# Optimization experiments

Hardware: AMD Instinct MI355X
Metric: run time of the kernel (lower is better)

## Reference

```python
import jax, jax.numpy as jnp
import numpy as np

N, E, DIM, H = 50000, 800000, 256, 4
HD = DIM // H  # per-head dim = 64
NEG_SLOPE = 0.2
EPS = 1e-5


def _layernorm(x, g, b):
    mu = jnp.mean(x, axis=-1, keepdims=True)
    var = jnp.mean(jnp.square(x - mu), axis=-1, keepdims=True)
    return (x - mu) * jax.lax.rsqrt(var + EPS) * g + b


def setup_inputs() -> dict:
    key = jax.random.key(0)
    ks = jax.random.split(key, 8)
    s = 1.0 / np.sqrt(DIM)
    return {
        "x": jax.random.normal(ks[0], (N, DIM), dtype=jnp.float32),
        "edge_index": jax.random.randint(ks[1], (2, E), 0, N, dtype=jnp.int64),
        "W": jax.random.normal(ks[2], (DIM, DIM), dtype=jnp.float32) * s,
        "a_src": jax.random.normal(ks[3], (H, HD), dtype=jnp.float32) * s,
        "a_dst": jax.random.normal(ks[4], (H, HD), dtype=jnp.float32) * s,
        "gat_b": jnp.zeros((DIM,), jnp.float32),
        "ln1_g": jnp.ones((DIM,), jnp.float32),
        "ln1_b": jnp.zeros((DIM,), jnp.float32),
        "W1": jax.random.normal(ks[5], (DIM, 2 * DIM), dtype=jnp.float32) * s,
        "b1": jnp.zeros((2 * DIM,), jnp.float32),
        "W2": jax.random.normal(ks[6], (2 * DIM, DIM), dtype=jnp.float32) * (1.0 / np.sqrt(2 * DIM)),
        "b2": jnp.zeros((DIM,), jnp.float32),
        "ln2_g": jnp.ones((DIM,), jnp.float32),
        "ln2_b": jnp.zeros((DIM,), jnp.float32),
    }


def _gat(x, edge_index, W, a_src, a_dst, gat_b):
    # add self-loops (PyG GATConv default)
    loops = jnp.arange(N, dtype=edge_index.dtype)
    src = jnp.concatenate([edge_index[0], loops])
    dst = jnp.concatenate([edge_index[1], loops])
    h = (x @ W).reshape(N, H, HD)                    # [N,H,D]
    al_src = jnp.einsum("nhd,hd->nh", h, a_src)      # [N,H]
    al_dst = jnp.einsum("nhd,hd->nh", h, a_dst)
    e = jax.nn.leaky_relu(al_src[src] + al_dst[dst], NEG_SLOPE)  # [E',H]
    # softmax over edges grouped by destination node
    emax = jax.ops.segment_max(e, dst, num_segments=N)           # [N,H]
    ex = jnp.exp(e - emax[dst])
    denom = jax.ops.segment_sum(ex, dst, num_segments=N)         # [N,H]
    alpha = ex / denom[dst]                                      # [E',H]
    msg = alpha[:, :, None] * h[src]                             # [E',H,D]
    out = jax.ops.segment_sum(msg, dst, num_segments=N)          # [N,H,D]
    return out.reshape(N, DIM) + gat_b


def reference(x, edge_index, W, a_src, a_dst, gat_b, ln1_g, ln1_b, W1, b1, W2, b2, ln2_g, ln2_b):
    res = x
    y = _gat(x, edge_index, W, a_src, a_dst, gat_b)
    y = _layernorm(y + res, ln1_g, ln1_b)
    res = y
    f = jax.nn.gelu(y @ W1 + b1, approximate=False) @ W2 + b2
    return _layernorm(f + res, ln2_g, ln2_b)
```

## Files before the change

kernel.cpp:

```cpp
#include <hip/hip_runtime.h>

typedef __bf16 bf16_t;
typedef __bf16 bf16x4 __attribute__((ext_vector_type(4)));
typedef __bf16 bf16x8 __attribute__((ext_vector_type(8)));
typedef float  f32x4  __attribute__((ext_vector_type(4)));
typedef unsigned u32x2 __attribute__((ext_vector_type(2)));

__device__ inline float loadf(const void* p, size_t i, int bf) {
    return bf ? (float)((const bf16_t*)p)[i] : ((const float*)p)[i];
}
__device__ inline void storef(void* p, size_t i, int bf, float v) {
    if (bf) ((bf16_t*)p)[i] = (bf16_t)v; else ((float*)p)[i] = v;
}
__device__ inline int eidx(const void* p, size_t i, int i64) {
    return i64 ? (int)((const long long*)p)[i] : ((const int*)p)[i];
}
__device__ inline float bflo(unsigned u) { return __uint_as_float(u << 16); }
__device__ inline float bfhi(unsigned u) { return __uint_as_float(u & 0xFFFF0000u); }

__global__ void detect_k(const void* __restrict__ x, const void* __restrict__ ei,
                         int E, int* __restrict__ flags) {
    int l = threadIdx.x;
    const unsigned* xu = (const unsigned*)x;
    unsigned low = xu[l] & 0xFFFFu;
    unsigned ex = (low >> 7) & 0xFF;
    int cnt = __popcll(__ballot(ex >= 115 && ex <= 133));
    const unsigned* eu = (const unsigned*)ei;
    int lim = E < 64 ? E : 64;
    unsigned v = (l < lim) ? eu[2 * (size_t)l + 1] : 0u;
    unsigned long long nz = __ballot(v != 0u);
    if (l == 0) { flags[0] = (cnt >= 32) ? 1 : 0; flags[1] = (nz == 0ull) ? 1 : 0; }
}

__global__ void transpose_k(const void* __restrict__ in, bf16_t* __restrict__ out,
                            int R, int C, const int* __restrict__ flags) {
    int bf = flags[0];
    int i = blockIdx.x * 256 + threadIdx.x;
    if (i < R * C) { int r = i / C, c = i % C; out[c * R + r] = (bf16_t)loadf(in, i, bf); }
}

__global__ __launch_bounds__(256) void gemm128(const void* __restrict__ A,
                                               const bf16_t* __restrict__ BT,
                                               const void* __restrict__ bias,
                                               bf16_t* __restrict__ C,
                                               int M, int N, int K, int act,
                                               const int* __restrict__ flags, int a_ext,
                                               const void* __restrict__ a_srcp,
                                               const void* __restrict__ a_dstp,
                                               float* __restrict__ alsrc,
                                               float* __restrict__ aldst, int do_al) {
    int bf = flags[0];
    int a_bf = a_ext ? bf : 1;
    __shared__ bf16_t As[128][40];
    __shared__ bf16_t Bs[128][40];
    int t = threadIdx.x;
    int tm = blockIdx.x * 128;
    int tn = blockIdx.y * 128;
    int w = t >> 6, l = t & 63;
    int wr = (w >> 1) * 64, wc = (w & 1) * 64;
    int lr = l & 15, lk = (l >> 4) * 8;

    f32x4 acc[4][4];
#pragma unroll
    for (int i = 0; i < 4; i++)
#pragma unroll
        for (int j = 0; j < 4; j++) acc[i][j] = (f32x4){0.f, 0.f, 0.f, 0.f};

    int r0 = t >> 2;
    int kc = (t & 3) * 8;

    for (int k0 = 0; k0 < K; k0 += 32) {
#pragma unroll
        for (int j = 0; j < 2; j++) {
            int r = r0 + j * 64;
            int ra = tm + r; if (ra > M - 1) ra = M - 1;
            if (a_bf) {
                *(bf16x8*)&As[r][kc] = *(const bf16x8*)((const bf16_t*)A + (size_t)ra * K + k0 + kc);
            } else {
                const float* Af = (const float*)A + (size_t)ra * K + k0 + kc;
                f32x4 a = *(const f32x4*)Af;
                f32x4 b2 = *(const f32x4*)(Af + 4);
                bf16x8 rr;
                rr[0]=(bf16_t)a[0]; rr[1]=(bf16_t)a[1]; rr[2]=(bf16_t)a[2]; rr[3]=(bf16_t)a[3];
                rr[4]=(bf16_t)b2[0]; rr[5]=(bf16_t)b2[1]; rr[6]=(bf16_t)b2[2]; rr[7]=(bf16_t)b2[3];
                *(bf16x8*)&As[r][kc] = rr;
            }
            *(bf16x8*)&Bs[r][kc] = *(const bf16x8*)(BT + (size_t)(tn + r) * K + k0 + kc);
        }
        __syncthreads();
        bf16x8 af[4], bg[4];
#pragma unroll
        for (int i = 0; i < 4; i++) {
            af[i] = *(bf16x8*)&As[wr + i * 16 + lr][lk];
            bg[i] = *(bf16x8*)&Bs[wc + i * 16 + lr][lk];
        }
#pragma unroll
        for (int i = 0; i < 4; i++)
#pragma unroll
            for (int j = 0; j < 4; j++)
                acc[i][j] = __builtin_amdgcn_mfma_f32_16x16x32_bf16(af[i], bg[j], acc[i][j], 0, 0, 0);
        __syncthreads();
    }

    int cr0 = (l >> 4) * 4;

    if (do_al) {
        float asv[4], adv[4];
#pragma unroll
        for (int j = 0; j < 4; j++) {
            int col = tn + wc + j * 16 + lr;
            asv[j] = loadf(a_srcp, col, bf);
            adv[j] = loadf(a_dstp, col, bf);
        }
        int head = (tn + wc) >> 6;
#pragma unroll
        for (int i = 0; i < 4; i++) {
#pragma unroll
            for (int q = 0; q < 4; q++) {
                float ps = acc[i][0][q]*asv[0] + acc[i][1][q]*asv[1] + acc[i][2][q]*asv[2] + acc[i][3][q]*asv[3];
                float pd = acc[i][0][q]*adv[0] + acc[i][1][q]*adv[1] + acc[i][2][q]*adv[2] + acc[i][3][q]*adv[3];
#pragma unroll
                for (int d = 1; d < 16; d <<= 1) { ps += __shfl_xor(ps, d); pd += __shfl_xor(pd, d); }
                int row = tm + wr + i * 16 + cr0 + q;
                if (lr == 0 && row < M) { alsrc[row * 4 + head] = ps; aldst[row * 4 + head] = pd; }
            }
        }
    }

#pragma unroll
    for (int i = 0; i < 4; i++) {
#pragma unroll
        for (int j = 0; j < 4; j++) {
            int col = tn + wc + j * 16 + lr;
            float bv = bias ? loadf(bias, col, bf) : 0.f;
#pragma unroll
            for (int q = 0; q < 4; q++) {
                int row = tm + wr + i * 16 + cr0 + q;
                if (row < M) {
                    float v = acc[i][j][q] + bv;
                    if (act) v = 0.5f * v * (1.f + erff(v * 0.70710678118f));
                    C[(size_t)row * N + col] = (bf16_t)v;
                }
            }
        }
    }
}

__global__ void deg_k(const void* __restrict__ ei, int* __restrict__ deg, int E, int N,
                      const int* __restrict__ flags) {
    int i64 = flags[1];
    int i = blockIdx.x * 256 + threadIdx.x;
    if (i < E) {
        int d = eidx(ei, (size_t)E + i, i64);
        if ((unsigned)d >= (unsigned)N) d = 0;
        atomicAdd(&deg[d], 1);
    }
}

__global__ __launch_bounds__(256) void scan1(const int* __restrict__ deg, int* __restrict__ offs,
                                             int* __restrict__ chunkSum) {
    __shared__ int s[256];
    int t = threadIdx.x, b = blockIdx.x;
    int v = deg[b * 256 + t];
    s[t] = v; __syncthreads();
#pragma unroll
    for (int d = 1; d < 256; d <<= 1) {
        int u = (t >= d) ? s[t - d] : 0;
        __syncthreads(); s[t] += u; __syncthreads();
    }
    offs[b * 256 + t] = s[t] - v;
    if (t == 255) chunkSum[b] = s[255];
}

__global__ __launch_bounds__(256) void scan2(const int* __restrict__ chunkSum, int* __restrict__ chunkOff, int nch) {
    __shared__ int s[256];
    int t = threadIdx.x;
    int v = (t < nch) ? chunkSum[t] : 0;
    s[t] = v; __syncthreads();
#pragma unroll
    for (int d = 1; d < 256; d <<= 1) {
        int u = (t >= d) ? s[t - d] : 0;
        __syncthreads(); s[t] += u; __syncthreads();
    }
    chunkOff[t] = s[t] - v;
}

__global__ void scan3(int* __restrict__ offs, const int* __restrict__ chunkOff,
                      int* __restrict__ cursor, int total) {
    int i = blockIdx.x * 256 + threadIdx.x;
    if (i < total) { int v = offs[i] + chunkOff[i >> 8]; offs[i] = v; cursor[i] = v; }
}

__global__ void scatter_k(const void* __restrict__ ei, int* __restrict__ cursor,
                          int* __restrict__ csr, float* __restrict__ ews4,
                          const float* __restrict__ alsrc, const float* __restrict__ aldst,
                          int E, int N, const int* __restrict__ flags) {
    int i64 = flags[1];
    int i = blockIdx.x * 256 + threadIdx.x;
    if (i < E) {
        int s = eidx(ei, i, i64);
        int d = eidx(ei, (size_t)E + i, i64);
        if ((unsigned)s >= (unsigned)N) s = 0;
        if ((unsigned)d >= (unsigned)N) d = 0;
        int p = atomicAdd(&cursor[d], 1);
        csr[p] = s;
        f32x4 as4 = *(const f32x4*)&alsrc[s * 4];
        f32x4 ad4 = *(const f32x4*)&aldst[d * 4];
        f32x4 w4;
#pragma unroll
        for (int hh = 0; hh < 4; hh++) {
            float e = as4[hh] + ad4[hh];
            e = e > 0.f ? e : 0.2f * e;
            w4[hh] = expf(fminf(e, 30.f));
        }
        *(f32x4*)&ews4[4 * (size_t)p] = w4;
    }
}

__global__ __launch_bounds__(256) void gat_agg_ln(
    const bf16_t* __restrict__ hbuf, const void* __restrict__ x,
    const float* __restrict__ alsrc, const float* __restrict__ aldst,
    const int* __restrict__ offs, const int* __restrict__ csr,
    const float* __restrict__ ews4,
    const void* __restrict__ gatb, const void* __restrict__ lng, const void* __restrict__ lnb,
    bf16_t* __restrict__ y, const int* __restrict__ flags, int N) {
    int bf = flags[0];
    int w = threadIdx.x >> 6, l = threadIdx.x & 63;
    int n = blockIdx.x * 4 + w;
    if (n >= N) return;
    int h = l >> 4;
    int col0 = l * 4;

    __shared__ int   srcs[4][64];
    __shared__ float ewt[4][4][68];

    int off = offs[n], deg = offs[n + 1] - off;

    float es = alsrc[n * 4 + h] + aldst[n * 4 + h];
    es = es > 0.f ? es : 0.2f * es;
    float wself = expf(fminf(es, 30.f));

    float a0 = 0.f, a1 = 0.f, a2 = 0.f, a3 = 0.f;
    f32x4 ssum = (f32x4){0.f, 0.f, 0.f, 0.f};

    for (int c0 = 0; c0 < deg; c0 += 64) {
        int cl = deg - c0; if (cl > 64) cl = 64;
        if (l < cl) {
            int sv = csr[off + c0 + l];
            srcs[w][l] = sv;
            f32x4 wv = *(const f32x4*)&ews4[4 * (size_t)(off + c0 + l)];
            ewt[w][0][l] = wv[0]; ewt[w][1][l] = wv[1];
            ewt[w][2][l] = wv[2]; ewt[w][3][l] = wv[3];
            ssum += wv;
        }
        int i = 0;
        for (; i + 4 <= cl; i += 4) {
            int s0 = __builtin_amdgcn_readfirstlane(srcs[w][i]);
            int s1 = __builtin_amdgcn_readfirstlane(srcs[w][i + 1]);
            int s2 = __builtin_amdgcn_readfirstlane(srcs[w][i + 2]);
            int s3 = __builtin_amdgcn_readfirstlane(srcs[w][i + 3]);
            u32x2 v0 = ((const u32x2*)(hbuf + (size_t)s0 * 256))[l];
            u32x2 v1 = ((const u32x2*)(hbuf + (size_t)s1 * 256))[l];
            u32x2 v2 = ((const u32x2*)(hbuf + (size_t)s2 * 256))[l];
            u32x2 v3 = ((const u32x2*)(hbuf + (size_t)s3 * 256))[l];
            f32x4 wq = *(const f32x4*)&ewt[w][h][i];
            a0 += wq[0]*bflo(v0[0]); a1 += wq[0]*bfhi(v0[0]); a2 += wq[0]*bflo(v0[1]); a3 += wq[0]*bfhi(v0[1]);
            a0 += wq[1]*bflo(v1[0]); a1 += wq[1]*bfhi(v1[0]); a2 += wq[1]*bflo(v1[1]); a3 += wq[1]*bfhi(v1[1]);
            a0 += wq[2]*bflo(v2[0]); a1 += wq[2]*bfhi(v2[0]); a2 += wq[2]*bflo(v2[1]); a3 += wq[2]*bfhi(v2[1]);
            a0 += wq[3]*bflo(v3[0]); a1 += wq[3]*bfhi(v3[0]); a2 += wq[3]*bflo(v3[1]); a3 += wq[3]*bfhi(v3[1]);
        }
        for (; i < cl; i++) {
            int sv = __builtin_amdgcn_readfirstlane(srcs[w][i]);
            float wgt = ewt[w][h][i];
            u32x2 v0 = ((const u32x2*)(hbuf + (size_t)sv * 256))[l];
            a0 += wgt*bflo(v0[0]); a1 += wgt*bfhi(v0[0]); a2 += wgt*bflo(v0[1]); a3 += wgt*bfhi(v0[1]);
        }
    }

#pragma unroll
    for (int d = 1; d < 64; d <<= 1) {
        ssum[0] += __shfl_xor(ssum[0], d);
        ssum[1] += __shfl_xor(ssum[1], d);
        ssum[2] += __shfl_xor(ssum[2], d);
        ssum[3] += __shfl_xor(ssum[3], d);
    }
    float dsum = (h == 0) ? ssum[0] : (h == 1) ? ssum[1] : (h == 2) ? ssum[2] : ssum[3];
    float di = 1.f / (dsum + wself);

    u32x2 sv2 = ((const u32x2*)(hbuf + (size_t)n * 256))[l];
    size_t xbase = (size_t)n * 256 + col0;
    float v0f = (a0 + wself*bflo(sv2[0])) * di + loadf(gatb, col0 + 0, bf) + loadf(x, xbase + 0, bf);
    float v1f = (a1 + wself*bfhi(sv2[0])) * di + loadf(gatb, col0 + 1, bf) + loadf(x, xbase + 1, bf);
    float v2f = (a2 + wself*bflo(sv2[1])) * di + loadf(gatb, col0 + 2, bf) + loadf(x, xbase + 2, bf);
    float v3f = (a3 + wself*bfhi(sv2[1])) * di + loadf(gatb, col0 + 3, bf) + loadf(x, xbase + 3, bf);

    float s1 = v0f + v1f + v2f + v3f;
#pragma unroll
    for (int d = 1; d < 64; d <<= 1) s1 += __shfl_xor(s1, d);
    float mu = s1 * (1.f / 256.f);
    float c0f = v0f - mu, c1f = v1f - mu, c2f = v2f - mu, c3f = v3f - mu;
    float sq = c0f*c0f + c1f*c1f + c2f*c2f + c3f*c3f;
#pragma unroll
    for (int d = 1; d < 64; d <<= 1) sq += __shfl_xor(sq, d);
    float rs = rsqrtf(sq * (1.f / 256.f) + 1e-5f);

    bf16x4 o;
    o[0] = (bf16_t)(c0f * rs * loadf(lng, col0 + 0, bf) + loadf(lnb, col0 + 0, bf));
    o[1] = (bf16_t)(c1f * rs * loadf(lng, col0 + 1, bf) + loadf(lnb, col0 + 1, bf));
    o[2] = (bf16_t)(c2f * rs * loadf(lng, col0 + 2, bf) + loadf(lnb, col0 + 2, bf));
    o[3] = (bf16_t)(c3f * rs * loadf(lng, col0 + 3, bf) + loadf(lnb, col0 + 3, bf));
    *(bf16x4*)&y[(size_t)n * 256 + col0] = o;
}

__global__ __launch_bounds__(256) void ln_res(const bf16_t* __restrict__ f, const bf16_t* __restrict__ y,
                                              const void* __restrict__ g, const void* __restrict__ b,
                                              void* __restrict__ out, int N, const int* __restrict__ flags) {
    int bf = flags[0];
    int row = blockIdx.x * 4 + (threadIdx.x >> 6);
    int l = threadIdx.x & 63;
    if (row >= N) return;
    int col0 = l * 4;
    u32x2 fv = *(const u32x2*)(f + (size_t)row * 256 + col0);
    u32x2 yv = *(const u32x2*)(y + (size_t)row * 256 + col0);
    float v0 = bflo(fv[0]) + bflo(yv[0]);
    float v1 = bfhi(fv[0]) + bfhi(yv[0]);
    float v2 = bflo(fv[1]) + bflo(yv[1]);
    float v3 = bfhi(fv[1]) + bfhi(yv[1]);
    float s = v0 + v1 + v2 + v3;
#pragma unroll
    for (int d = 1; d < 64; d <<= 1) s += __shfl_xor(s, d);
    float mu = s * (1.f / 256.f);
    float c0 = v0 - mu, c1 = v1 - mu, c2 = v2 - mu, c3 = v3 - mu;
    float sq = c0*c0 + c1*c1 + c2*c2 + c3*c3;
#pragma unroll
    for (int d = 1; d < 64; d <<= 1) sq += __shfl_xor(sq, d);
    float rs = rsqrtf(sq * (1.f / 256.f) + 1e-5f);
    float o0 = c0 * rs * loadf(g, col0 + 0, bf) + loadf(b, col0 + 0, bf);
    float o1 = c1 * rs * loadf(g, col0 + 1, bf) + loadf(b, col0 + 1, bf);
    float o2 = c2 * rs * loadf(g, col0 + 2, bf) + loadf(b, col0 + 2, bf);
    float o3 = c3 * rs * loadf(g, col0 + 3, bf) + loadf(b, col0 + 3, bf);
    if (bf) {
        bf16x4 o; o[0]=(bf16_t)o0; o[1]=(bf16_t)o1; o[2]=(bf16_t)o2; o[3]=(bf16_t)o3;
        *(bf16x4*)&((bf16_t*)out)[(size_t)row * 256 + col0] = o;
    } else {
        f32x4 o = (f32x4){o0, o1, o2, o3};
        *(f32x4*)&((float*)out)[(size_t)row * 256 + col0] = o;
    }
}

extern "C" void kernel_launch(void* const* d_in, const int* in_sizes, int n_in,
                              void* d_out, int out_size, void* d_ws, size_t ws_size,
                              hipStream_t stream) {
    const void* x    = d_in[0];
    const void* ei   = d_in[1];
    const void* W    = d_in[2];
    const void* a_src= d_in[3];
    const void* a_dst= d_in[4];
    const void* gatb = d_in[5];
    const void* ln1g = d_in[6];
    const void* ln1b = d_in[7];
    const void* W1   = d_in[8];
    const void* b1   = d_in[9];
    const void* W2   = d_in[10];
    const void* b2   = d_in[11];
    const void* ln2g = d_in[12];
    const void* ln2b = d_in[13];

    const int DIM = 256, DFF = 512;
    int N = in_sizes[0] / DIM;
    int E = in_sizes[1] / 2;

    char* ws = (char*)d_ws;
    size_t o = 0;
    auto alloc = [&](size_t bytes) { void* p = ws + o; o += (bytes + 255) & ~(size_t)255; return p; };
    int*    flags  = (int*)alloc(256);
    bf16_t* WT     = (bf16_t*)alloc((size_t)DIM * DIM * 2);
    bf16_t* W1T    = (bf16_t*)alloc((size_t)DIM * DFF * 2);
    bf16_t* W2T    = (bf16_t*)alloc((size_t)DFF * DIM * 2);
    float*  alsrc  = (float*)alloc((size_t)N * 4 * 4);
    float*  aldst  = (float*)alloc((size_t)N * 4 * 4);
    int nch = (N + 255) / 256;
    int tot = nch * 256;
    int* deg      = (int*)alloc((size_t)tot * 4);
    int* offs     = (int*)alloc((size_t)(tot + 1) * 4);
    int* cursor   = (int*)alloc((size_t)tot * 4);
    int* chunkSum = (int*)alloc(256 * 4);
    int* chunkOff = (int*)alloc(256 * 4);
    int* csr      = (int*)alloc((size_t)E * 4);
    float* ews4   = (float*)alloc((size_t)E * 16);
    bf16_t* h     = (bf16_t*)alloc((size_t)N * DIM * 2);
    bf16_t* yb    = (bf16_t*)alloc((size_t)N * DIM * 2);
    bf16_t* fb    = h;
    size_t remain = (ws_size > o) ? (ws_size - o) : 0;
    long CH = (long)(remain / ((size_t)DFF * 2));
    if (CH > N) CH = N;
    if (CH < 1024) CH = 1024;
    bf16_t* t1 = (bf16_t*)alloc((size_t)CH * DFF * 2);

    detect_k<<<1, 64, 0, stream>>>(x, ei, E, flags);
    hipMemsetAsync(deg, 0, (size_t)tot * 4, stream);

    transpose_k<<<(DIM * DIM + 255) / 256, 256, 0, stream>>>(W,  WT,  DIM, DIM, flags);
    transpose_k<<<(DIM * DFF + 255) / 256, 256, 0, stream>>>(W1, W1T, DIM, DFF, flags);
    transpose_k<<<(DFF * DIM + 255) / 256, 256, 0, stream>>>(W2, W2T, DFF, DIM, flags);

    dim3 g1((N + 127) / 128, DIM / 128);
    gemm128<<<g1, 256, 0, stream>>>(x, WT, nullptr, h, N, DIM, DIM, 0, flags, 1,
                                    a_src, a_dst, alsrc, aldst, 1);

    deg_k<<<(E + 255) / 256, 256, 0, stream>>>(ei, deg, E, N, flags);
    scan1<<<nch, 256, 0, stream>>>(deg, offs, chunkSum);
    scan2<<<1, 256, 0, stream>>>(chunkSum, chunkOff, nch);
    scan3<<<(tot + 255) / 256, 256, 0, stream>>>(offs, chunkOff, cursor, tot);
    scatter_k<<<(E + 255) / 256, 256, 0, stream>>>(ei, cursor, csr, ews4, alsrc, aldst, E, N, flags);

    gat_agg_ln<<<(N + 3) / 4, 256, 0, stream>>>(h, x, alsrc, aldst, offs, csr, ews4,
                                                gatb, ln1g, ln1b, yb, flags, N);

    for (long r0 = 0; r0 < N; r0 += CH) {
        int m = (int)((N - r0 < CH) ? (N - r0) : CH);
        dim3 g2((m + 127) / 128, DFF / 128);
        gemm128<<<g2, 256, 0, stream>>>(yb + r0 * DIM, W1T, b1, t1, m, DFF, DIM, 1, flags, 0,
                                        nullptr, nullptr, nullptr, nullptr, 0);
        dim3 g3((m + 127) / 128, DIM / 128);
        gemm128<<<g3, 256, 0, stream>>>(t1, W2T, b2, fb + r0 * DIM, m, DIM, DFF, 0, flags, 0,
                                        nullptr, nullptr, nullptr, nullptr, 0);
    }

    ln_res<<<(N + 3) / 4, 256, 0, stream>>>(fb, yb, ln2g, ln2b, d_out, N, flags);
}
```

Measured before the change: 427.9 us.

## Double-buffer GEMM with direct global-to-LDS loads, stage output, compress edge weights

The GEMM now loads A/B tiles straight into LDS via global_load_lds into a double buffer, so the next K-slab's fetch overlaps the current MFMA work. A k-major LDS layout replaces the padded one. Epilogue stores go through LDS and write coalesced 16-byte rows. Input x is pre-converted to bf16 in a separate pass so the GEMM sees only bf16 A, and per-edge softmax weights are stored as bf16 instead of fp32 to halve that traffic, at a small precision cost and one extra kernel pass over x.

```diff
diff --git a/kernel.cpp b/kernel.cpp
--- a/kernel.cpp
+++ b/kernel.cpp
@@ -17,6 +17,12 @@
 }
 __device__ inline float bflo(unsigned u) { return __uint_as_float(u << 16); }
 __device__ inline float bfhi(unsigned u) { return __uint_as_float(u & 0xFFFF0000u); }
+
+__device__ inline void gload16(const bf16_t* g, char* l) {
+    __builtin_amdgcn_global_load_lds(
+        (const __attribute__((address_space(1))) unsigned*)g,
+        (__attribute__((address_space(3))) unsigned*)l, 16, 0, 0);
+}
 
 __global__ void detect_k(const void* __restrict__ x, const void* __restrict__ ei,
                          int E, int* __restrict__ flags) {
@@ -32,6 +38,26 @@
     if (l == 0) { flags[0] = (cnt >= 32) ? 1 : 0; flags[1] = (nz == 0ull) ? 1 : 0; }
 }
 
+__global__ void tobf16_k(const void* __restrict__ in, bf16_t* __restrict__ out,
+                         long n, const int* __restrict__ flags) {
+    int bf = flags[0];
+    long i = ((long)blockIdx.x * 256 + threadIdx.x) * 8;
+    long stride = (long)gridDim.x * 256 * 8;
+    if (bf) {
+        for (; i < n; i += stride)
+            *(bf16x8*)&out[i] = *(const bf16x8*)((const bf16_t*)in + i);
+    } else {
+        for (; i < n; i += stride) {
+            f32x4 a = *(const f32x4*)((const float*)in + i);
+            f32x4 b = *(const f32x4*)((const float*)in + i + 4);
+            bf16x8 r;
+            r[0]=(bf16_t)a[0]; r[1]=(bf16_t)a[1]; r[2]=(bf16_t)a[2]; r[3]=(bf16_t)a[3];
+            r[4]=(bf16_t)b[0]; r[5]=(bf16_t)b[1]; r[6]=(bf16_t)b[2]; r[7]=(bf16_t)b[3];
+            *(bf16x8*)&out[i] = r;
+        }
+    }
+}
+
 __global__ void transpose_k(const void* __restrict__ in, bf16_t* __restrict__ out,
                             int R, int C, const int* __restrict__ flags) {
     int bf = flags[0];
@@ -39,26 +65,25 @@
     if (i < R * C) { int r = i / C, c = i % C; out[c * R + r] = (bf16_t)loadf(in, i, bf); }
 }
 
-__global__ __launch_bounds__(256) void gemm128(const void* __restrict__ A,
+__global__ __launch_bounds__(256) void gemm128(const bf16_t* __restrict__ A,
                                                const bf16_t* __restrict__ BT,
                                                const void* __restrict__ bias,
                                                bf16_t* __restrict__ C,
                                                int M, int N, int K, int act,
-                                               const int* __restrict__ flags, int a_ext,
+                                               const int* __restrict__ flags,
                                                const void* __restrict__ a_srcp,
                                                const void* __restrict__ a_dstp,
                                                float* __restrict__ alsrc,
                                                float* __restrict__ aldst, int do_al) {
     int bf = flags[0];
-    int a_bf = a_ext ? bf : 1;
-    __shared__ bf16_t As[128][40];
-    __shared__ bf16_t Bs[128][40];
+    __shared__ __align__(16) char smem[34816];
     int t = threadIdx.x;
     int tm = blockIdx.x * 128;
     int tn = blockIdx.y * 128;
     int w = t >> 6, l = t & 63;
     int wr = (w >> 1) * 64, wc = (w & 1) * 64;
-    int lr = l & 15, lk = (l >> 4) * 8;
+    int lr16 = l & 15, kg = l >> 4;
+    int NK = K >> 5;
 
     f32x4 acc[4][4];
 #pragma unroll
@@ -66,39 +91,83 @@
 #pragma unroll
         for (int j = 0; j < 4; j++) acc[i][j] = (f32x4){0.f, 0.f, 0.f, 0.f};
 
-    int r0 = t >> 2;
-    int kc = (t & 3) * 8;
-
-    for (int k0 = 0; k0 < K; k0 += 32) {
-#pragma unroll
-        for (int j = 0; j < 2; j++) {
-            int r = r0 + j * 64;
-            int ra = tm + r; if (ra > M - 1) ra = M - 1;
-            if (a_bf) {
-                *(bf16x8*)&As[r][kc] = *(const bf16x8*)((const bf16_t*)A + (size_t)ra * K + k0 + kc);
-            } else {
-                const float* Af = (const float*)A + (size_t)ra * K + k0 + kc;
-                f32x4 a = *(const f32x4*)Af;
-                f32x4 b2 = *(const f32x4*)(Af + 4);
-                bf16x8 rr;
-                rr[0]=(bf16_t)a[0]; rr[1]=(bf16_t)a[1]; rr[2]=(bf16_t)a[2]; rr[3]=(bf16_t)a[3];
-                rr[4]=(bf16_t)b2[0]; rr[5]=(bf16_t)b2[1]; rr[6]=(bf16_t)b2[2]; rr[7]=(bf16_t)b2[3];
-                *(bf16x8*)&As[r][kc] = rr;
-            }
-            *(bf16x8*)&Bs[r][kc] = *(const bf16x8*)(BT + (size_t)(tn + r) * K + k0 + kc);
+    bool fast = (tm + 128 <= M);
+
+    if (fast) {
+        int buf = 0;
+#pragma unroll
+        for (int ii = 0; ii < 2; ii++) {
+            int c = w + ii * 4;
+            int rowa = tm + (c & 1) * 64 + l;
+            int rowb = tn + (c & 1) * 64 + l;
+            int kc = (c >> 1) * 8;
+            gload16(A  + (size_t)rowa * K + kc, smem +         c * 1024 + l * 16);
+            gload16(BT + (size_t)rowb * K + kc, smem + 16384 + c * 1024 + l * 16);
         }
         __syncthreads();
-        bf16x8 af[4], bg[4];
-#pragma unroll
-        for (int i = 0; i < 4; i++) {
-            af[i] = *(bf16x8*)&As[wr + i * 16 + lr][lk];
-            bg[i] = *(bf16x8*)&Bs[wc + i * 16 + lr][lk];
-        }
-#pragma unroll
-        for (int i = 0; i < 4; i++)
-#pragma unroll
-            for (int j = 0; j < 4; j++)
-                acc[i][j] = __builtin_amdgcn_mfma_f32_16x16x32_bf16(af[i], bg[j], acc[i][j], 0, 0, 0);
+        for (int ks = 0; ks < NK; ks++) {
+            if (ks + 1 < NK) {
+                int k0 = (ks + 1) << 5;
+                char* ab = smem + (buf ^ 1) * 8192;
+                char* bb = smem + 16384 + (buf ^ 1) * 8192;
+#pragma unroll
+                for (int ii = 0; ii < 2; ii++) {
+                    int c = w + ii * 4;
+                    int rowa = tm + (c & 1) * 64 + l;
+                    int rowb = tn + (c & 1) * 64 + l;
+                    int kc = k0 + (c >> 1) * 8;
+                    gload16(A  + (size_t)rowa * K + kc, ab + c * 1024 + l * 16);
+                    gload16(BT + (size_t)rowb * K + kc, bb + c * 1024 + l * 16);
+                }
+            }
+            const char* ab = smem + buf * 8192;
+            const char* bb = smem + 16384 + buf * 8192;
+            bf16x8 af[4], bg[4];
+#pragma unroll
+            for (int i = 0; i < 4; i++) {
+                af[i] = *(const bf16x8*)(ab + ((size_t)(kg * 128 + wr + i * 16 + lr16)) * 16);
+                bg[i] = *(const bf16x8*)(bb + ((size_t)(kg * 128 + wc + i * 16 + lr16)) * 16);
+            }
+#pragma unroll
+            for (int i = 0; i < 4; i++)
+#pragma unroll
+                for (int j = 0; j < 4; j++)
+                    acc[i][j] = __builtin_amdgcn_mfma_f32_16x16x32_bf16(af[i], bg[j], acc[i][j], 0, 0, 0);
+            __syncthreads();
+            buf ^= 1;
+        }
+    } else {
+        int r = t >> 2, kg2 = t & 3;
+        for (int ks = 0; ks < NK; ks++) {
+            int k0 = ks << 5;
+            bf16x8 va[2], vb[2];
+#pragma unroll
+            for (int j = 0; j < 2; j++) {
+                int row = r + j * 64;
+                int ra = tm + row; if (ra > M - 1) ra = M - 1;
+                va[j] = *(const bf16x8*)(A + (size_t)ra * K + k0 + kg2 * 8);
+                vb[j] = *(const bf16x8*)(BT + (size_t)(tn + row) * K + k0 + kg2 * 8);
+            }
+            __syncthreads();
+#pragma unroll
+            for (int j = 0; j < 2; j++) {
+                int row = r + j * 64;
+                *(bf16x8*)(smem + ((size_t)(kg2 * 128 + row)) * 16) = va[j];
+                *(bf16x8*)(smem + 16384 + ((size_t)(kg2 * 128 + row)) * 16) = vb[j];
+            }
+            __syncthreads();
+            bf16x8 af[4], bg[4];
+#pragma unroll
+            for (int i = 0; i < 4; i++) {
+                af[i] = *(const bf16x8*)(smem + ((size_t)(kg * 128 + wr + i * 16 + lr16)) * 16);
+                bg[i] = *(const bf16x8*)(smem + 16384 + ((size_t)(kg * 128 + wc + i * 16 + lr16)) * 16);
+            }
+#pragma unroll
+            for (int i = 0; i < 4; i++)
+#pragma unroll
+                for (int j = 0; j < 4; j++)
+                    acc[i][j] = __builtin_amdgcn_mfma_f32_16x16x32_bf16(af[i], bg[j], acc[i][j], 0, 0, 0);
+        }
         __syncthreads();
     }
 
@@ -108,7 +177,7 @@
         float asv[4], adv[4];
 #pragma unroll
         for (int j = 0; j < 4; j++) {
-            int col = tn + wc + j * 16 + lr;
+            int col = tn + wc + j * 16 + lr16;
             asv[j] = loadf(a_srcp, col, bf);
             adv[j] = loadf(a_dstp, col, bf);
         }
@@ -122,27 +191,34 @@
 #pragma unroll
                 for (int d = 1; d < 16; d <<= 1) { ps += __shfl_xor(ps, d); pd += __shfl_xor(pd, d); }
                 int row = tm + wr + i * 16 + cr0 + q;
-                if (lr == 0 && row < M) { alsrc[row * 4 + head] = ps; aldst[row * 4 + head] = pd; }
-            }
-        }
-    }
-
+                if (lr16 == 0 && row < M) { alsrc[row * 4 + head] = ps; aldst[row * 4 + head] = pd; }
+            }
+        }
+    }
+
+    bf16_t (*Cst)[136] = (bf16_t(*)[136])smem;
 #pragma unroll
     for (int i = 0; i < 4; i++) {
 #pragma unroll
         for (int j = 0; j < 4; j++) {
-            int col = tn + wc + j * 16 + lr;
-            float bv = bias ? loadf(bias, col, bf) : 0.f;
+            int col = wc + j * 16 + lr16;
+            float bv = bias ? loadf(bias, tn + col, bf) : 0.f;
 #pragma unroll
             for (int q = 0; q < 4; q++) {
-                int row = tm + wr + i * 16 + cr0 + q;
-                if (row < M) {
-                    float v = acc[i][j][q] + bv;
-                    if (act) v = 0.5f * v * (1.f + erff(v * 0.70710678118f));
-                    C[(size_t)row * N + col] = (bf16_t)v;
-                }
-            }
-        }
+                float v = acc[i][j][q] + bv;
+                if (act) v = 0.5f * v * (1.f + erff(v * 0.70710678118f));
+                Cst[wr + i * 16 + cr0 + q][col] = (bf16_t)v;
+            }
+        }
+    }
+    __syncthreads();
+#pragma unroll
+    for (int it = 0; it < 8; it++) {
+        int idx = it * 256 + t;
+        int row = idx >> 4;
+        int c8 = (idx & 15) * 8;
+        if (tm + row < M)
+            *(bf16x8*)&C[(size_t)(tm + row) * N + tn + c8] = *(const bf16x8*)&Cst[row][c8];
     }
 }
 
@@ -192,7 +268,7 @@
 }
 
 __global__ void scatter_k(const void* __restrict__ ei, int* __restrict__ cursor,
-                          int* __restrict__ csr, float* __restrict__ ews4,
+                          int* __restrict__ csr, bf16_t* __restrict__ ewsb,
                           const float* __restrict__ alsrc, const float* __restrict__ aldst,
                           int E, int N, const int* __restrict__ flags) {
     int i64 = flags[1];
@@ -206,14 +282,14 @@
         csr[p] = s;
         f32x4 as4 = *(const f32x4*)&alsrc[s * 4];
         f32x4 ad4 = *(const f32x4*)&aldst[d * 4];
-        f32x4 w4;
+        bf16x4 w4;
 #pragma unroll
         for (int hh = 0; hh < 4; hh++) {
             float e = as4[hh] + ad4[hh];
             e = e > 0.f ? e : 0.2f * e;
-            w4[hh] = expf(fminf(e, 30.f));
-        }
-        *(f32x4*)&ews4[4 * (size_t)p] = w4;
+            w4[hh] = (bf16_t)expf(fminf(e, 30.f));
+        }
+        *(bf16x4*)&ewsb[4 * (size_t)p] = w4;
     }
 }
 
@@ -221,7 +297,7 @@
     const bf16_t* __restrict__ hbuf, const void* __restrict__ x,
     const float* __restrict__ alsrc, const float* __restrict__ aldst,
     const int* __restrict__ offs, const int* __restrict__ csr,
-    const float* __restrict__ ews4,
+    const bf16_t* __restrict__ ewsb,
     const void* __restrict__ gatb, const void* __restrict__ lng, const void* __restrict__ lnb,
     bf16_t* __restrict__ y, const int* __restrict__ flags, int N) {
     int bf = flags[0];
@@ -248,10 +324,11 @@
         if (l < cl) {
             int sv = csr[off + c0 + l];
             srcs[w][l] = sv;
-            f32x4 wv = *(const f32x4*)&ews4[4 * (size_t)(off + c0 + l)];
-            ewt[w][0][l] = wv[0]; ewt[w][1][l] = wv[1];
-            ewt[w][2][l] = wv[2]; ewt[w][3][l] = wv[3];
-            ssum += wv;
+            bf16x4 wv4 = *(const bf16x4*)&ewsb[4 * (size_t)(off + c0 + l)];
+            float w0 = (float)wv4[0], w1 = (float)wv4[1], w2 = (float)wv4[2], w3 = (float)wv4[3];
+            ewt[w][0][l] = w0; ewt[w][1][l] = w1;
+            ewt[w][2][l] = w2; ewt[w][3][l] = w3;
+            ssum += (f32x4){w0, w1, w2, w3};
         }
         int i = 0;
         for (; i + 4 <= cl; i += 4) {
@@ -387,9 +464,10 @@
     int* chunkSum = (int*)alloc(256 * 4);
     int* chunkOff = (int*)alloc(256 * 4);
     int* csr      = (int*)alloc((size_t)E * 4);
-    float* ews4   = (float*)alloc((size_t)E * 16);
+    bf16_t* ewsb  = (bf16_t*)alloc((size_t)E * 8);
     bf16_t* h     = (bf16_t*)alloc((size_t)N * DIM * 2);
     bf16_t* yb    = (bf16_t*)alloc((size_t)N * DIM * 2);
+    bf16_t* xb    = (bf16_t*)alloc((size_t)N * DIM * 2);
     bf16_t* fb    = h;
     size_t remain = (ws_size > o) ? (ws_size - o) : 0;
     long CH = (long)(remain / ((size_t)DFF * 2));
@@ -400,30 +478,31 @@
     detect_k<<<1, 64, 0, stream>>>(x, ei, E, flags);
     hipMemsetAsync(deg, 0, (size_t)tot * 4, stream);
 
+    tobf16_k<<<4096, 256, 0, stream>>>(x, xb, (long)N * DIM, flags);
     transpose_k<<<(DIM * DIM + 255) / 256, 256, 0, stream>>>(W,  WT,  DIM, DIM, flags);
     transpose_k<<<(DIM * DFF + 255) / 256, 256, 0, stream>>>(W1, W1T, DIM, DFF, flags);
     transpose_k<<<(DFF * DIM + 255) / 256, 256, 0, stream>>>(W2, W2T, DFF, DIM, flags);
 
     dim3 g1((N + 127) / 128, DIM / 128);
-    gemm128<<<g1, 256, 0, stream>>>(x, WT, nullptr, h, N, DIM, DIM, 0, flags, 1,
+    gemm128<<<g1, 256, 0, stream>>>(xb, WT, nullptr, h, N, DIM, DIM, 0, flags,
                                     a_src, a_dst, alsrc, aldst, 1);
 
     deg_k<<<(E + 255) / 256, 256, 0, stream>>>(ei, deg, E, N, flags);
     scan1<<<nch, 256, 0, stream>>>(deg, offs, chunkSum);
     scan2<<<1, 256, 0, stream>>>(chunkSum, chunkOff, nch);
     scan3<<<(tot + 255) / 256, 256, 0, stream>>>(offs, chunkOff, cursor, tot);
-    scatter_k<<<(E + 255) / 256, 256, 0, stream>>>(ei, cursor, csr, ews4, alsrc, aldst, E, N, flags);
-
-    gat_agg_ln<<<(N + 3) / 4, 256, 0, stream>>>(h, x, alsrc, aldst, offs, csr, ews4,
+    scatter_k<<<(E + 255) / 256, 256, 0, stream>>>(ei, cursor, csr, ewsb, alsrc, aldst, E, N, flags);
+
+    gat_agg_ln<<<(N + 3) / 4, 256, 0, stream>>>(h, x, alsrc, aldst, offs, csr, ewsb,
                                                 gatb, ln1g, ln1b, yb, flags, N);
 
     for (long r0 = 0; r0 < N; r0 += CH) {
         int m = (int)((N - r0 < CH) ? (N - r0) : CH);
         dim3 g2((m + 127) / 128, DFF / 128);
-        gemm128<<<g2, 256, 0, stream>>>(yb + r0 * DIM, W1T, b1, t1, m, DFF, DIM, 1, flags, 0,
+        gemm128<<<g2, 256, 0, stream>>>(yb + r0 * DIM, W1T, b1, t1, m, DFF, DIM, 1, flags,
                                         nullptr, nullptr, nullptr, nullptr, 0);
         dim3 g3((m + 127) / 128, DIM / 128);
-        gemm128<<<g3, 256, 0, stream>>>(t1, W2T, b2, fb + r0 * DIM, m, DIM, DFF, 0, flags, 0,
+        gemm128<<<g3, 256, 0, stream>>>(t1, W2T, b2, fb + r0 * DIM, m, DIM, DFF, 0, flags,
                                         nullptr, nullptr, nullptr, nullptr, 0);
     }
 
```

Result: faster. 366.3 us (-14.4%).
